# Performance work log

Measured on AMD Instinct MI355X. Metric: run time of the kernel, lower is better.

## Reference

```python
import jax, jax.numpy as jnp
import numpy as np

N_LEVELS = 16
F_PER_LEVEL = 2
LOG2_T = 19
TABLE = 1 << LOG2_T
BASE_RES = 16.0
FINEST_RES = 512.0
PRIMES = jnp.array([1, 2654435761, 805459861, 3674653429, 2097192037, 1434869437], dtype=jnp.uint32)
# Hashing offsets: BOX_OFFSETS_6D enumerates dim0 in the OUTERMOST loop -> dim d uses bit (5-d) of vertex index.
OFF_HASH = jnp.array(((np.arange(64)[:, None] >> (5 - np.arange(6))) & 1).astype(np.int32))
# Interpolation weights use LSB-first bits (vertex_binary = [i >> d & 1]) -- faithful to the source (incl. its bit-order mismatch).
OFF_W = jnp.array(((np.arange(64)[:, None] >> np.arange(6)) & 1).astype(np.bool_))


def _hash6(coords):
    # coords: [..., 6] int32 -> int32 indices in [0, 2^19). uint32 wraparound matches torch int32 overflow + bitmask.
    u = coords.astype(jnp.uint32) * PRIMES
    h = u[..., 0]
    for d in range(1, 6):
        h = h ^ u[..., d]
    return (h & jnp.uint32(TABLE - 1)).astype(jnp.int32)


def _encode_level(emb, res, x):
    # emb: [T, F], res: scalar resolution, x: [B, 6] clamped to [0,1] box
    grid = 1.0 / res
    bl = jnp.floor(x * res).astype(jnp.int32)            # bottom-left voxel index, [B, 6]
    vmin = bl.astype(x.dtype) * grid                     # voxel_min_vertex
    w = jnp.clip((x - vmin) / (grid + 1e-6), 0.0, 1.0)   # [B, 6]
    verts = bl[:, None, :] + OFF_HASH[None]              # [B, 64, 6]
    ve = emb[_hash6(verts)]                              # gather: [B, 64, F]
    wv = jnp.where(OFF_W[None], w[:, None, :], 1.0 - w[:, None, :]).prod(-1)  # [B, 64]
    return jnp.einsum('bv,bvf->bf', wv, ve)


def hash_encode(x, embeddings):
    b = np.exp((np.log(FINEST_RES) - np.log(BASE_RES)) / (N_LEVELS - 1))
    res = jnp.maximum(jnp.floor(BASE_RES * b ** jnp.arange(N_LEVELS, dtype=jnp.float32)), 1.0)
    xc = jnp.clip(x, 0.0, 1.0)

    def body(carry, lv):
        emb, r = lv
        return carry, _encode_level(emb, r, xc)

    _, feats = jax.lax.scan(body, 0, (embeddings, res))  # [L, B, F]
    return jnp.transpose(feats, (1, 0, 2)).reshape(x.shape[0], N_LEVELS * F_PER_LEVEL)


def _mlp(W0, b0, Wres, bres, scales, Wout, bout, h):
    # NeRF_MLP_Residual_Scaled: initial -> (num_layers-1) scaled residual blocks -> output
    h = jax.nn.relu(h @ W0 + b0)
    for i in range(Wres.shape[0]):
        h = scales[i] * jax.nn.relu(h @ Wres[i] + bres[i]) + h
    return h @ Wout + bout


def setup_inputs() -> dict:
    key = jax.random.key(0)
    ks = jax.random.split(key, 10)
    B, C, H, IN, OUT = 524288, 4, 256, 32, 1
    NB = 3  # num_layers - 1 residual blocks
    x = jax.random.uniform(ks[0], (B, 6), jnp.float32)
    layer_id = jax.random.randint(ks[1], (B,), 0, C)
    embeddings = jax.random.uniform(ks[2], (N_LEVELS, TABLE, F_PER_LEVEL), jnp.float32, -1e-4, 1e-4)
    W0 = jax.random.normal(ks[3], (C, IN, H), jnp.float32) / np.sqrt(IN)
    b0 = jax.random.normal(ks[4], (C, H), jnp.float32) * 0.01
    Wres = jax.random.normal(ks[5], (C, NB, H, H), jnp.float32) / np.sqrt(H)
    bres = jax.random.normal(ks[6], (C, NB, H), jnp.float32) * 0.01
    scales = jax.random.normal(ks[7], (C, NB), jnp.float32) * 0.1
    Wout = jax.random.normal(ks[8], (C, H, OUT), jnp.float32) / np.sqrt(H)
    bout = jax.random.normal(ks[9], (C, OUT), jnp.float32) * 0.01
    return dict(x_6d_input=x, layer_id=layer_id, embeddings=embeddings, W0=W0, b0=b0,
                Wres=Wres, bres=bres, scales=scales, Wout=Wout, bout=bout)


def reference(x_6d_input, layer_id, embeddings, W0, b0, Wres, bres, scales, Wout, bout):
    enc = hash_encode(x_6d_input, embeddings)  # [B, 32]
    outs = jax.vmap(_mlp, in_axes=(0, 0, 0, 0, 0, 0, 0, None))(W0, b0, Wres, bres, scales, Wout, bout, enc)  # [C, B, out]
    midx = (layer_id % outs.shape[0]).astype(jnp.int32)
    return jnp.take_along_axis(outs, midx[None, :, None], axis=0)[0]  # [B, out]
```

## Files before the change

### kernel.cpp

```cpp
#include <hip/hip_runtime.h>
#include <stdint.h>

#define HTABLE (1u << 19)
#define TMASK  (HTABLE - 1u)
#define TILE   64
#define KSTR   264
#define KE     40

#define NTILE   8196
#define NCHUNK  2049
#define BPAD    (NCHUNK * 256)

typedef __attribute__((ext_vector_type(8))) short short8;
typedef __attribute__((ext_vector_type(4))) float floatx4;

__device__ __forceinline__ float relu_(float v) { return fmaxf(v, 0.f); }

__device__ __forceinline__ uint32_t f2bf(float f) {
    uint32_t u = __float_as_uint(f);
    return (u + 0x7FFFu + ((u >> 16) & 1u)) >> 16;
}

__device__ __forceinline__ uint32_t sel4(const uint4& v, uint32_t i) {
    uint32_t lo = (i & 1u) ? v.y : v.x;
    uint32_t hi = (i & 1u) ? v.w : v.z;
    return (i & 2u) ? hi : lo;
}

__device__ __constant__ uint32_t PRS[6] = {1u, 2654435761u, 805459861u, 3674653429u, 2097192037u, 1434869437u};
__device__ __constant__ float RESF[16]  = {16.f,20.f,25.f,32.f,40.f,50.f,64.f,80.f,101.f,128.f,161.f,203.f,256.f,322.f,406.f,512.f};
__device__ __constant__ float GRIDF[16] = {1.f/16.f,1.f/20.f,1.f/25.f,1.f/32.f,1.f/40.f,1.f/50.f,1.f/64.f,1.f/80.f,
                                           1.f/101.f,1.f/128.f,1.f/161.f,1.f/203.f,1.f/256.f,1.f/322.f,1.f/406.f,1.f/512.f};

__global__ void k_count(const int* __restrict__ lid, int n, int* __restrict__ cnt) {
    __shared__ int h4[4];
    int i = blockIdx.x * blockDim.x + threadIdx.x;
    if (threadIdx.x < 4) h4[threadIdx.x] = 0;
    __syncthreads();
    if (i < n) atomicAdd(&h4[lid[i] & 3], 1);
    __syncthreads();
    if (threadIdx.x < 4) atomicAdd(&cnt[threadIdx.x], h4[threadIdx.x]);
}

__global__ void k_offsets(const int* __restrict__ cnt, int* __restrict__ cursor) {
    if (threadIdx.x == 0 && blockIdx.x == 0) {
        int off = 0;
        for (int k = 0; k < 4; k++) {
            cursor[k] = off;
            off = (off + cnt[k] + 63) & ~63;
        }
    }
}

__global__ void k_scatter(const int* __restrict__ lid, const float* __restrict__ x, int n,
                          int* __restrict__ cursor, int* __restrict__ perm, float* __restrict__ xp) {
    int i = blockIdx.x * blockDim.x + threadIdx.x;
    if (i >= n) return;
    int lane = threadIdx.x & 63;
    int c = lid[i] & 3;
    unsigned long long m0 = __ballot(c == 0), m1 = __ballot(c == 1);
    unsigned long long m2 = __ballot(c == 2), m3 = __ballot(c == 3);
    unsigned long long mc = (c == 0) ? m0 : (c == 1) ? m1 : (c == 2) ? m2 : m3;
    int rank = __popcll(mc & ((1ull << lane) - 1ull));
    int cntl = (lane == 0) ? __popcll(m0) : (lane == 1) ? __popcll(m1) : (lane == 2) ? __popcll(m2) : __popcll(m3);
    int basev = 0;
    if (lane < 4) basev = atomicAdd(&cursor[lane], cntl);
    int base = __shfl(basev, c, 64);
    int dst = base + rank;
    perm[dst] = i;
    const float2* xr = (const float2*)(x + (size_t)i * 6);
    float2* xw = (float2*)(xp + (size_t)dst * 6);
    float2 a = xr[0], b = xr[1], cc = xr[2];
    xw[0] = a; xw[1] = b; xw[2] = cc;
}

__global__ __launch_bounds__(256) void k_packtab(const float* __restrict__ emb, uint32_t* __restrict__ T) {
    const int i = blockIdx.x * 256 + threadIdx.x;
    float2 e = ((const float2*)emb)[i];
    T[i] = f2bf(e.x) | (f2bf(e.y) << 16);
}

__global__ __launch_bounds__(256) void k_prep(const float* __restrict__ Wres, const float* __restrict__ W0,
                                              uint16_t* __restrict__ Wrt, uint16_t* __restrict__ W0t) {
    __shared__ float sm[64 * 65 > 32 * 257 ? 64 * 65 : 32 * 257];
    const int t = threadIdx.x;
    const int bid = blockIdx.x;
    if (bid < 192) {
        const int c = bid / 48, rem = bid % 48, ib = rem / 16, tile = rem % 16;
        const int n0 = (tile / 4) * 64, k0 = (tile % 4) * 64;
        const float* src = Wres + (size_t)(c * 3 + ib) * 65536;
        for (int i = 0; i < 16; i++) {
            int idx = t + 256 * i, r = idx >> 6, cc = idx & 63;
            sm[r * 65 + cc] = src[(size_t)(k0 + r) * 256 + n0 + cc];
        }
        __syncthreads();
        uint16_t* dst = Wrt + (size_t)(c * 3 + ib) * 65536;
        for (int i = 0; i < 16; i++) {
            int idx = t + 256 * i, rn = idx >> 6, ck = idx & 63;
            dst[(size_t)(n0 + rn) * 256 + k0 + ck] = (uint16_t)f2bf(sm[ck * 65 + rn]);
        }
    } else {
        const int c = bid - 192;
        for (int i = 0; i < 32; i++) {
            int idx = t + 256 * i, k = idx >> 8, n = idx & 255;
            sm[k * 257 + n] = W0[(size_t)c * 8192 + idx];
        }
        __syncthreads();
        for (int i = 0; i < 32; i++) {
            int idx = t + 256 * i, n = idx >> 5, k = idx & 31;
            W0t[(size_t)c * 8192 + idx] = (uint16_t)f2bf(sm[k * 257 + n]);
        }
    }
}

__global__ __launch_bounds__(256, 4) void k_encode(
    const float* __restrict__ xp, const uint32_t* __restrict__ T,
    uint32_t* __restrict__ encP)
{
    __shared__ float xs[256 * 6];
    const int t = threadIdx.x;
    const int NC8 = NCHUNK * 8;
    const int pass = (blockIdx.x >= NC8) ? 1 : 0;
    const int rem  = blockIdx.x - pass * NC8;
    const int l    = (rem & 7) + (pass << 3);
    const int chunk = rem >> 3;
    const int pbase = chunk << 8;

    for (int idx = t; idx < 256 * 6; idx += 256) {
        float v = xp[(size_t)pbase * 6 + idx];
        xs[idx] = fminf(fmaxf(v, 0.f), 1.f);
    }
    __syncthreads();

    const float res  = RESF[l];
    const float grid = GRIDF[l];
    float wv[6]; uint32_t ua[6], ub[6];
    #pragma unroll
    for (int d = 0; d < 6; d++) {
        float xv  = xs[t * 6 + d];
        float blf = floorf(xv * res);
        float w   = (xv - blf * grid) / (grid + 1e-6f);
        wv[d] = fminf(fmaxf(w, 0.f), 1.f);
        uint32_t uu = (uint32_t)(int)blf * PRS[d];
        ua[d] = uu; ub[d] = uu + PRS[d];
    }
    uint32_t HK[4]; float WK[4];
    #pragma unroll
    for (int q = 0; q < 4; q++) {
        const int b1 = (q >> 1) & 1, bb = q & 1;
        HK[q] = (b1 ? ub[4] : ua[4]) ^ (bb ? ub[5] : ua[5]);
        WK[q] = (bb ? wv[0] : 1.f - wv[0]) * (b1 ? wv[1] : 1.f - wv[1]);
    }
    uint32_t S8[8]; float W8[8];
    #pragma unroll
    for (int jj = 0; jj < 8; jj++) {
        const int j1 = jj >> 2, j = jj & 3;
        const int b1 = (j >> 1) & 1, bb = j & 1;
        const uint32_t hj = (b1 ? ub[2] : ua[2]) ^ (bb ? ub[3] : ua[3]);
        const float  wj = ((bb ? wv[2] : 1.f - wv[2]) * (b1 ? wv[3] : 1.f - wv[3]));
        S8[jj] = (j1 ? ub[1] : ua[1]) ^ hj;
        W8[jj] = (j1 ? wv[4] : 1.f - wv[4]) * wj;
    }
    const float w5a = 1.f - wv[5], w5b = wv[5];
    const uint32_t bl0  = ua[0];
    const uint32_t mask = bl0 ^ (bl0 + 1u);
    const uint32_t* __restrict__ Tl  = T + (size_t)l * HTABLE;
    const uint4*    __restrict__ Tl4 = reinterpret_cast<const uint4*>(Tl);

    float f0 = 0.f, f1 = 0.f;
    #pragma unroll 2
    for (int jj = 0; jj < 8; jj++) {
        const uint32_t Sj = S8[jj];
        const float   wj = W8[jj];
        #pragma unroll
        for (int k = 0; k < 4; k++) {
            const uint32_t h  = (bl0 ^ Sj ^ HK[k]) & TMASK;
            const float wS = wj * WK[k];
            uint32_t pa, pb;
            if (mask == 1u) {
                const uint2 pr = *(const uint2*)(Tl + (h & ~1u));
                pa = (h & 1u) ? pr.y : pr.x;
                pb = (h & 1u) ? pr.x : pr.y;
            } else if (mask == 3u) {
                const uint4 La = Tl4[h >> 2];
                const uint32_t i0 = h & 3u;
                pa = sel4(La, i0);
                pb = sel4(La, i0 ^ 3u);
            } else {
                pa = Tl[h];
                pb = Tl[h ^ mask];
            }
            const float e0x = __uint_as_float(pa << 16),  e0y = __uint_as_float(pa & 0xFFFF0000u);
            const float e1x = __uint_as_float(pb << 16),  e1y = __uint_as_float(pb & 0xFFFF0000u);
            f0 = fmaf(wS, fmaf(w5a, e0x, w5b * e1x), f0);
            f1 = fmaf(wS, fmaf(w5a, e0y, w5b * e1y), f1);
        }
    }
    const uint32_t val = f2bf(f0) | (f2bf(f1) << 16);
    __builtin_nontemporal_store(val, &encP[(size_t)l * BPAD + pbase + t]);
}

__global__ __launch_bounds__(512, 4) void k_mlp2(
    const int* __restrict__ lid, const uint32_t* __restrict__ encP,
    const uint16_t* __restrict__ W0t, const float* __restrict__ b0,
    const uint16_t* __restrict__ Wrt, const float* __restrict__ bres,
    const float* __restrict__ scales, const float* __restrict__ Wout, const float* __restrict__ bout,
    const int* __restrict__ perm, float* __restrict__ out)
{
    __shared__ uint16_t hB[64 * KSTR];
    __shared__ __align__(16) char smU[64 * KE * 2];
    __shared__ float    bs[256];
    __shared__ int      permL[TILE];
    uint16_t* encB = (uint16_t*)smU;
    float*    outP = (float*)smU;

    const int t  = threadIdx.x;
    const int lane = t & 63;
    const int wv = t >> 6;
    const int mi = lane & 15;
    const int q  = lane >> 4;

    if (t < TILE) permL[t] = perm[(size_t)blockIdx.x * TILE + t];
    __syncthreads();
    const int g0 = permL[0];
    if (g0 < 0) return;
    const int c = lid[g0] & 3;

    if (t < 256) bs[t] = b0[c * 256 + t];
    for (int idx = t; idx < 16 * 64; idx += 512) {
        const int l = idx >> 6, pp = idx & 63;
        ((uint32_t*)encB)[pp * (KE / 2) + l] =
            __builtin_nontemporal_load(&encP[(size_t)l * BPAD + (size_t)blockIdx.x * TILE + pp]);
    }
    __syncthreads();

    floatx4 acc[2][4];
    floatx4 h_reg[2][4];

    {
        #pragma unroll
        for (int mt = 0; mt < 2; mt++)
            #pragma unroll
            for (int nt = 0; nt < 4; nt++) acc[mt][nt] = (floatx4){0.f, 0.f, 0.f, 0.f};
        const short8* Wp = (const short8*)(W0t + (size_t)c * 8192);
        short8 A[2], Bf[4];
        #pragma unroll
        for (int mt = 0; mt < 2; mt++) A[mt] = Wp[(wv * 32 + mt * 16 + mi) * 4 + q];
        #pragma unroll
        for (int nt = 0; nt < 4; nt++) Bf[nt] = *(const short8*)&encB[(nt * 16 + mi) * KE + q * 8];
        #pragma unroll
        for (int mt = 0; mt < 2; mt++)
            #pragma unroll
            for (int nt = 0; nt < 4; nt++)
                acc[mt][nt] = __builtin_amdgcn_mfma_f32_16x16x32_bf16(A[mt], Bf[nt], acc[mt][nt], 0, 0, 0);
        #pragma unroll
        for (int mt = 0; mt < 2; mt++) {
            const int nb = wv * 32 + mt * 16 + q * 4;
            #pragma unroll
            for (int nt = 0; nt < 4; nt++) {
                floatx4 u = acc[mt][nt], h;
                h[0] = relu_(u[0] + bs[nb + 0]); h[1] = relu_(u[1] + bs[nb + 1]);
                h[2] = relu_(u[2] + bs[nb + 2]); h[3] = relu_(u[3] + bs[nb + 3]);
                h_reg[mt][nt] = h;
                uint2 pk; pk.x = f2bf(h[0]) | (f2bf(h[1]) << 16); pk.y = f2bf(h[2]) | (f2bf(h[3]) << 16);
                *(uint2*)&hB[(nt * 16 + mi) * KSTR + nb] = pk;
            }
        }
    }
    __syncthreads();

    #pragma unroll 1
    for (int ib = 0; ib < 3; ib++) {
        if (t < 256) bs[t] = bres[(size_t)((c * 3 + ib) << 8) + t];
        const float s = scales[c * 3 + ib];
        #pragma unroll
        for (int mt = 0; mt < 2; mt++)
            #pragma unroll
            for (int nt = 0; nt < 4; nt++) acc[mt][nt] = (floatx4){0.f, 0.f, 0.f, 0.f};

        const short8* Wp = (const short8*)(Wrt + (size_t)(c * 3 + ib) * 65536);
        short8 Acur[2], Anext[2], Bf[4];
        #pragma unroll
        for (int mt = 0; mt < 2; mt++) Acur[mt] = Wp[(wv * 32 + mt * 16 + mi) * 32 + q];
        #pragma unroll 1
        for (int ks = 0; ks < 8; ks++) {
            #pragma unroll
            for (int nt = 0; nt < 4; nt++)
                Bf[nt] = *(const short8*)&hB[(nt * 16 + mi) * KSTR + ks * 32 + q * 8];
            if (ks < 7) {
                #pragma unroll
                for (int mt = 0; mt < 2; mt++)
                    Anext[mt] = Wp[(wv * 32 + mt * 16 + mi) * 32 + (ks + 1) * 4 + q];
            }
            #pragma unroll
            for (int mt = 0; mt < 2; mt++)
                #pragma unroll
                for (int nt = 0; nt < 4; nt++)
                    acc[mt][nt] = __builtin_amdgcn_mfma_f32_16x16x32_bf16(Acur[mt], Bf[nt], acc[mt][nt], 0, 0, 0);
            #pragma unroll
            for (int mt = 0; mt < 2; mt++) Acur[mt] = Anext[mt];
        }
        __syncthreads();
        #pragma unroll
        for (int mt = 0; mt < 2; mt++) {
            const int nb = wv * 32 + mt * 16 + q * 4;
            #pragma unroll
            for (int nt = 0; nt < 4; nt++) {
                floatx4 u = acc[mt][nt];
                floatx4 h = h_reg[mt][nt];
                h[0] = fmaf(s, relu_(u[0] + bs[nb + 0]), h[0]);
                h[1] = fmaf(s, relu_(u[1] + bs[nb + 1]), h[1]);
                h[2] = fmaf(s, relu_(u[2] + bs[nb + 2]), h[2]);
                h[3] = fmaf(s, relu_(u[3] + bs[nb + 3]), h[3]);
                h_reg[mt][nt] = h;
                if (ib < 2) {
                    uint2 pk; pk.x = f2bf(h[0]) | (f2bf(h[1]) << 16); pk.y = f2bf(h[2]) | (f2bf(h[3]) << 16);
                    *(uint2*)&hB[(nt * 16 + mi) * KSTR + nb] = pk;
                }
            }
        }
        if (ib < 2) __syncthreads();
    }

    __syncthreads();
    if (t < 256) bs[t] = Wout[c * 256 + t];
    __syncthreads();
    float po[4] = {0.f, 0.f, 0.f, 0.f};
    #pragma unroll
    for (int mt = 0; mt < 2; mt++) {
        const int nb = wv * 32 + mt * 16 + q * 4;
        const float w0v = bs[nb + 0], w1v = bs[nb + 1], w2v = bs[nb + 2], w3v = bs[nb + 3];
        #pragma unroll
        for (int nt = 0; nt < 4; nt++) {
            const floatx4 h = h_reg[mt][nt];
            po[nt] += h[0] * w0v + h[1] * w1v + h[2] * w2v + h[3] * w3v;
        }
    }
    #pragma unroll
    for (int nt = 0; nt < 4; nt++) {
        float v = po[nt];
        v += __shfl_xor(v, 16, 64);
        v += __shfl_xor(v, 32, 64);
        if (q == 0) outP[wv * 64 + nt * 16 + mi] = v;
    }
    __syncthreads();
    if (t < TILE) {
        float r = outP[t]       + outP[64 + t]  + outP[128 + t] + outP[192 + t]
                + outP[256 + t] + outP[320 + t] + outP[384 + t] + outP[448 + t] + bout[c];
        const int gi = permL[t];
        if (gi >= 0) out[gi] = r;
    }
}

extern "C" void kernel_launch(void* const* d_in, const int* in_sizes, int n_in,
                              void* d_out, int out_size, void* d_ws, size_t ws_size,
                              hipStream_t stream) {
    const float* x      = (const float*)d_in[0];
    const int*   lid    = (const int*)  d_in[1];
    const float* emb    = (const float*)d_in[2];
    const float* W0     = (const float*)d_in[3];
    const float* b0     = (const float*)d_in[4];
    const float* Wres   = (const float*)d_in[5];
    const float* bres   = (const float*)d_in[6];
    const float* scales = (const float*)d_in[7];
    const float* Wout   = (const float*)d_in[8];
    const float* bout   = (const float*)d_in[9];
    float* out = (float*)d_out;

    const int B = in_sizes[1];
    int* cnt    = (int*)d_ws;
    int* cursor = cnt + 4;
    int*      perm = (int*)((char*)d_ws + 16384);
    uint16_t* W0t  = (uint16_t*)((char*)d_ws + 2228224);
    uint16_t* Wrt  = (uint16_t*)((char*)d_ws + 2359296);
    uint32_t* encP = (uint32_t*)((char*)d_ws + (4ull  << 20));
    uint32_t* T    = (uint32_t*)((char*)d_ws + (38ull << 20));
    float*    xp   = (float*)   ((char*)d_ws + (70ull << 20));

    (void)hipMemsetAsync(d_ws, 0, 64, stream);
    (void)hipMemsetAsync(perm, 0xFF, (size_t)NTILE * TILE * sizeof(int), stream);
    k_packtab<<<(16 * (int)HTABLE) / 256, 256, 0, stream>>>(emb, T);
    k_prep   <<<196, 256, 0, stream>>>(Wres, W0, Wrt, W0t);
    k_count  <<<B / 256, 256, 0, stream>>>(lid, B, cnt);
    k_offsets<<<1, 64, 0, stream>>>(cnt, cursor);
    k_scatter<<<B / 256, 256, 0, stream>>>(lid, x, B, cursor, perm, xp);
    k_encode <<<NCHUNK * 16, 256, 0, stream>>>(xp, T, encP);
    k_mlp2   <<<NTILE, 512, 0, stream>>>(lid, encP, W0t, b0, Wrt, bres, scales, Wout, bout, perm, out);
}
```

Measured before the change: 1.742 ms.

## Fuse prep kernels into one launch and retile MLP waves as 4x2 fragments

Merges the table packing, weight transposition, class counting and perm memset into a single kernel, so several launches and a memset become one launch. In the MLP kernel each wave now covers 64 output features by 32 points (4x2 MFMA tiles) instead of 32x64 (2x4). That doubles the weight fragments per wave and halves the activation fragments read from LDS. The partial output reduction changes to four partials per point, read as one float4. The fused kernel hardcodes block counts (COUNT_N 2048) that assume a fixed batch size, and the larger A-fragment set raises register pressure.

```diff
diff --git a/kernel.cpp b/kernel.cpp
--- a/kernel.cpp
+++ b/kernel.cpp
@@ -11,6 +11,11 @@
 #define NCHUNK  2049
 #define BPAD    (NCHUNK * 256)
 
+#define PACK_N  32768
+#define PREP_N  196
+#define COUNT_N 2048
+#define PERM_N  2049
+
 typedef __attribute__((ext_vector_type(8))) short short8;
 typedef __attribute__((ext_vector_type(4))) float floatx4;
 
@@ -32,14 +37,64 @@
 __device__ __constant__ float GRIDF[16] = {1.f/16.f,1.f/20.f,1.f/25.f,1.f/32.f,1.f/40.f,1.f/50.f,1.f/64.f,1.f/80.f,
                                            1.f/101.f,1.f/128.f,1.f/161.f,1.f/203.f,1.f/256.f,1.f/322.f,1.f/406.f,1.f/512.f};
 
-__global__ void k_count(const int* __restrict__ lid, int n, int* __restrict__ cnt) {
-    __shared__ int h4[4];
-    int i = blockIdx.x * blockDim.x + threadIdx.x;
-    if (threadIdx.x < 4) h4[threadIdx.x] = 0;
-    __syncthreads();
-    if (i < n) atomicAdd(&h4[lid[i] & 3], 1);
-    __syncthreads();
-    if (threadIdx.x < 4) atomicAdd(&cnt[threadIdx.x], h4[threadIdx.x]);
+__global__ __launch_bounds__(256) void k_fusedprep(
+    const float* __restrict__ emb, uint32_t* __restrict__ T,
+    const float* __restrict__ Wres, const float* __restrict__ W0,
+    uint16_t* __restrict__ Wrt, uint16_t* __restrict__ W0t,
+    const int* __restrict__ lid, int n, int* __restrict__ cnt,
+    int* __restrict__ perm)
+{
+    const int t = threadIdx.x;
+    const int bid = blockIdx.x;
+    if (bid < PACK_N) {
+        const int i = bid * 256 + t;
+        float2 e = ((const float2*)emb)[i];
+        T[i] = f2bf(e.x) | (f2bf(e.y) << 16);
+        return;
+    }
+    if (bid < PACK_N + PREP_N) {
+        __shared__ float sm[64 * 65 > 32 * 257 ? 64 * 65 : 32 * 257];
+        const int pb = bid - PACK_N;
+        if (pb < 192) {
+            const int c = pb / 48, rem = pb % 48, ib = rem / 16, tile = rem % 16;
+            const int n0 = (tile / 4) * 64, k0 = (tile % 4) * 64;
+            const float* src = Wres + (size_t)(c * 3 + ib) * 65536;
+            for (int i = 0; i < 16; i++) {
+                int idx = t + 256 * i, r = idx >> 6, cc = idx & 63;
+                sm[r * 65 + cc] = src[(size_t)(k0 + r) * 256 + n0 + cc];
+            }
+            __syncthreads();
+            uint16_t* dst = Wrt + (size_t)(c * 3 + ib) * 65536;
+            for (int i = 0; i < 16; i++) {
+                int idx = t + 256 * i, rn = idx >> 6, ck = idx & 63;
+                dst[(size_t)(n0 + rn) * 256 + k0 + ck] = (uint16_t)f2bf(sm[ck * 65 + rn]);
+            }
+        } else {
+            const int c = pb - 192;
+            for (int i = 0; i < 32; i++) {
+                int idx = t + 256 * i, k = idx >> 8, nn = idx & 255;
+                sm[k * 257 + nn] = W0[(size_t)c * 8192 + idx];
+            }
+            __syncthreads();
+            for (int i = 0; i < 32; i++) {
+                int idx = t + 256 * i, nn = idx >> 5, k = idx & 31;
+                W0t[(size_t)c * 8192 + idx] = (uint16_t)f2bf(sm[k * 257 + nn]);
+            }
+        }
+        return;
+    }
+    if (bid < PACK_N + PREP_N + COUNT_N) {
+        __shared__ int h4[4];
+        const int i = (bid - PACK_N - PREP_N) * 256 + t;
+        if (t < 4) h4[t] = 0;
+        __syncthreads();
+        if (i < n) atomicAdd(&h4[lid[i] & 3], 1);
+        __syncthreads();
+        if (t < 4) atomicAdd(&cnt[t], h4[t]);
+        return;
+    }
+    const int i = (bid - PACK_N - PREP_N - COUNT_N) * 256 + t;
+    if (i < NTILE * TILE) perm[i] = -1;
 }
 
 __global__ void k_offsets(const int* __restrict__ cnt, int* __restrict__ cursor) {
@@ -74,45 +129,6 @@
     xw[0] = a; xw[1] = b; xw[2] = cc;
 }
 
-__global__ __launch_bounds__(256) void k_packtab(const float* __restrict__ emb, uint32_t* __restrict__ T) {
-    const int i = blockIdx.x * 256 + threadIdx.x;
-    float2 e = ((const float2*)emb)[i];
-    T[i] = f2bf(e.x) | (f2bf(e.y) << 16);
-}
-
-__global__ __launch_bounds__(256) void k_prep(const float* __restrict__ Wres, const float* __restrict__ W0,
-                                              uint16_t* __restrict__ Wrt, uint16_t* __restrict__ W0t) {
-    __shared__ float sm[64 * 65 > 32 * 257 ? 64 * 65 : 32 * 257];
-    const int t = threadIdx.x;
-    const int bid = blockIdx.x;
-    if (bid < 192) {
-        const int c = bid / 48, rem = bid % 48, ib = rem / 16, tile = rem % 16;
-        const int n0 = (tile / 4) * 64, k0 = (tile % 4) * 64;
-        const float* src = Wres + (size_t)(c * 3 + ib) * 65536;
-        for (int i = 0; i < 16; i++) {
-            int idx = t + 256 * i, r = idx >> 6, cc = idx & 63;
-            sm[r * 65 + cc] = src[(size_t)(k0 + r) * 256 + n0 + cc];
-        }
-        __syncthreads();
-        uint16_t* dst = Wrt + (size_t)(c * 3 + ib) * 65536;
-        for (int i = 0; i < 16; i++) {
-            int idx = t + 256 * i, rn = idx >> 6, ck = idx & 63;
-            dst[(size_t)(n0 + rn) * 256 + k0 + ck] = (uint16_t)f2bf(sm[ck * 65 + rn]);
-        }
-    } else {
-        const int c = bid - 192;
-        for (int i = 0; i < 32; i++) {
-            int idx = t + 256 * i, k = idx >> 8, n = idx & 255;
-            sm[k * 257 + n] = W0[(size_t)c * 8192 + idx];
-        }
-        __syncthreads();
-        for (int i = 0; i < 32; i++) {
-            int idx = t + 256 * i, n = idx >> 5, k = idx & 31;
-            W0t[(size_t)c * 8192 + idx] = (uint16_t)f2bf(sm[k * 257 + n]);
-        }
-    }
-}
-
 __global__ __launch_bounds__(256, 4) void k_encode(
     const float* __restrict__ xp, const uint32_t* __restrict__ T,
     uint32_t* __restrict__ encP)
@@ -217,6 +233,8 @@
     const int t  = threadIdx.x;
     const int lane = t & 63;
     const int wv = t >> 6;
+    const int s  = wv >> 1;
+    const int ph = wv & 1;
     const int mi = lane & 15;
     const int q  = lane >> 4;
 
@@ -234,36 +252,36 @@
     }
     __syncthreads();
 
-    floatx4 acc[2][4];
-    floatx4 h_reg[2][4];
+    floatx4 acc[4][2];
+    floatx4 h_reg[4][2];
 
     {
         #pragma unroll
-        for (int mt = 0; mt < 2; mt++)
-            #pragma unroll
-            for (int nt = 0; nt < 4; nt++) acc[mt][nt] = (floatx4){0.f, 0.f, 0.f, 0.f};
+        for (int mt = 0; mt < 4; mt++)
+            #pragma unroll
+            for (int nt = 0; nt < 2; nt++) acc[mt][nt] = (floatx4){0.f, 0.f, 0.f, 0.f};
         const short8* Wp = (const short8*)(W0t + (size_t)c * 8192);
-        short8 A[2], Bf[4];
-        #pragma unroll
-        for (int mt = 0; mt < 2; mt++) A[mt] = Wp[(wv * 32 + mt * 16 + mi) * 4 + q];
-        #pragma unroll
-        for (int nt = 0; nt < 4; nt++) Bf[nt] = *(const short8*)&encB[(nt * 16 + mi) * KE + q * 8];
-        #pragma unroll
-        for (int mt = 0; mt < 2; mt++)
-            #pragma unroll
-            for (int nt = 0; nt < 4; nt++)
+        short8 A[4], Bf[2];
+        #pragma unroll
+        for (int mt = 0; mt < 4; mt++) A[mt] = Wp[(s * 64 + mt * 16 + mi) * 4 + q];
+        #pragma unroll
+        for (int nt = 0; nt < 2; nt++) Bf[nt] = *(const short8*)&encB[(ph * 32 + nt * 16 + mi) * KE + q * 8];
+        #pragma unroll
+        for (int mt = 0; mt < 4; mt++)
+            #pragma unroll
+            for (int nt = 0; nt < 2; nt++)
                 acc[mt][nt] = __builtin_amdgcn_mfma_f32_16x16x32_bf16(A[mt], Bf[nt], acc[mt][nt], 0, 0, 0);
         #pragma unroll
-        for (int mt = 0; mt < 2; mt++) {
-            const int nb = wv * 32 + mt * 16 + q * 4;
-            #pragma unroll
-            for (int nt = 0; nt < 4; nt++) {
+        for (int mt = 0; mt < 4; mt++) {
+            const int nb = s * 64 + mt * 16 + q * 4;
+            #pragma unroll
+            for (int nt = 0; nt < 2; nt++) {
                 floatx4 u = acc[mt][nt], h;
                 h[0] = relu_(u[0] + bs[nb + 0]); h[1] = relu_(u[1] + bs[nb + 1]);
                 h[2] = relu_(u[2] + bs[nb + 2]); h[3] = relu_(u[3] + bs[nb + 3]);
                 h_reg[mt][nt] = h;
                 uint2 pk; pk.x = f2bf(h[0]) | (f2bf(h[1]) << 16); pk.y = f2bf(h[2]) | (f2bf(h[3]) << 16);
-                *(uint2*)&hB[(nt * 16 + mi) * KSTR + nb] = pk;
+                *(uint2*)&hB[(ph * 32 + nt * 16 + mi) * KSTR + nb] = pk;
             }
         }
     }
@@ -272,50 +290,50 @@
     #pragma unroll 1
     for (int ib = 0; ib < 3; ib++) {
         if (t < 256) bs[t] = bres[(size_t)((c * 3 + ib) << 8) + t];
-        const float s = scales[c * 3 + ib];
-        #pragma unroll
-        for (int mt = 0; mt < 2; mt++)
-            #pragma unroll
-            for (int nt = 0; nt < 4; nt++) acc[mt][nt] = (floatx4){0.f, 0.f, 0.f, 0.f};
+        const float sc = scales[c * 3 + ib];
+        #pragma unroll
+        for (int mt = 0; mt < 4; mt++)
+            #pragma unroll
+            for (int nt = 0; nt < 2; nt++) acc[mt][nt] = (floatx4){0.f, 0.f, 0.f, 0.f};
 
         const short8* Wp = (const short8*)(Wrt + (size_t)(c * 3 + ib) * 65536);
-        short8 Acur[2], Anext[2], Bf[4];
-        #pragma unroll
-        for (int mt = 0; mt < 2; mt++) Acur[mt] = Wp[(wv * 32 + mt * 16 + mi) * 32 + q];
+        short8 Acur[4], Anext[4], Bf[2];
+        #pragma unroll
+        for (int mt = 0; mt < 4; mt++) Acur[mt] = Wp[(s * 64 + mt * 16 + mi) * 32 + q];
         #pragma unroll 1
         for (int ks = 0; ks < 8; ks++) {
             #pragma unroll
-            for (int nt = 0; nt < 4; nt++)
-                Bf[nt] = *(const short8*)&hB[(nt * 16 + mi) * KSTR + ks * 32 + q * 8];
+            for (int nt = 0; nt < 2; nt++)
+                Bf[nt] = *(const short8*)&hB[(ph * 32 + nt * 16 + mi) * KSTR + ks * 32 + q * 8];
             if (ks < 7) {
                 #pragma unroll
-                for (int mt = 0; mt < 2; mt++)
-                    Anext[mt] = Wp[(wv * 32 + mt * 16 + mi) * 32 + (ks + 1) * 4 + q];
-            }
-            #pragma unroll
-            for (int mt = 0; mt < 2; mt++)
+                for (int mt = 0; mt < 4; mt++)
+                    Anext[mt] = Wp[(s * 64 + mt * 16 + mi) * 32 + (ks + 1) * 4 + q];
+            }
+            #pragma unroll
+            for (int mt = 0; mt < 4; mt++)
                 #pragma unroll
-                for (int nt = 0; nt < 4; nt++)
+                for (int nt = 0; nt < 2; nt++)
                     acc[mt][nt] = __builtin_amdgcn_mfma_f32_16x16x32_bf16(Acur[mt], Bf[nt], acc[mt][nt], 0, 0, 0);
             #pragma unroll
-            for (int mt = 0; mt < 2; mt++) Acur[mt] = Anext[mt];
+            for (int mt = 0; mt < 4; mt++) Acur[mt] = Anext[mt];
         }
         __syncthreads();
         #pragma unroll
-        for (int mt = 0; mt < 2; mt++) {
-            const int nb = wv * 32 + mt * 16 + q * 4;
-            #pragma unroll
-            for (int nt = 0; nt < 4; nt++) {
+        for (int mt = 0; mt < 4; mt++) {
+            const int nb = s * 64 + mt * 16 + q * 4;
+            #pragma unroll
+            for (int nt = 0; nt < 2; nt++) {
                 floatx4 u = acc[mt][nt];
                 floatx4 h = h_reg[mt][nt];
-                h[0] = fmaf(s, relu_(u[0] + bs[nb + 0]), h[0]);
-                h[1] = fmaf(s, relu_(u[1] + bs[nb + 1]), h[1]);
-                h[2] = fmaf(s, relu_(u[2] + bs[nb + 2]), h[2]);
-                h[3] = fmaf(s, relu_(u[3] + bs[nb + 3]), h[3]);
+                h[0] = fmaf(sc, relu_(u[0] + bs[nb + 0]), h[0]);
+                h[1] = fmaf(sc, relu_(u[1] + bs[nb + 1]), h[1]);
+                h[2] = fmaf(sc, relu_(u[2] + bs[nb + 2]), h[2]);
+                h[3] = fmaf(sc, relu_(u[3] + bs[nb + 3]), h[3]);
                 h_reg[mt][nt] = h;
                 if (ib < 2) {
                     uint2 pk; pk.x = f2bf(h[0]) | (f2bf(h[1]) << 16); pk.y = f2bf(h[2]) | (f2bf(h[3]) << 16);
-                    *(uint2*)&hB[(nt * 16 + mi) * KSTR + nb] = pk;
+                    *(uint2*)&hB[(ph * 32 + nt * 16 + mi) * KSTR + nb] = pk;
                 }
             }
         }
@@ -325,28 +343,28 @@
     __syncthreads();
     if (t < 256) bs[t] = Wout[c * 256 + t];
     __syncthreads();
-    float po[4] = {0.f, 0.f, 0.f, 0.f};
+    float po[2] = {0.f, 0.f};
     #pragma unroll
-    for (int mt = 0; mt < 2; mt++) {
-        const int nb = wv * 32 + mt * 16 + q * 4;
+    for (int mt = 0; mt < 4; mt++) {
+        const int nb = s * 64 + mt * 16 + q * 4;
         const float w0v = bs[nb + 0], w1v = bs[nb + 1], w2v = bs[nb + 2], w3v = bs[nb + 3];
         #pragma unroll
-        for (int nt = 0; nt < 4; nt++) {
+        for (int nt = 0; nt < 2; nt++) {
             const floatx4 h = h_reg[mt][nt];
             po[nt] += h[0] * w0v + h[1] * w1v + h[2] * w2v + h[3] * w3v;
         }
     }
     #pragma unroll
-    for (int nt = 0; nt < 4; nt++) {
+    for (int nt = 0; nt < 2; nt++) {
         float v = po[nt];
         v += __shfl_xor(v, 16, 64);
         v += __shfl_xor(v, 32, 64);
-        if (q == 0) outP[wv * 64 + nt * 16 + mi] = v;
+        if (q == 0) outP[(ph * 32 + nt * 16 + mi) * 4 + s] = v;
     }
     __syncthreads();
     if (t < TILE) {
-        float r = outP[t]       + outP[64 + t]  + outP[128 + t] + outP[192 + t]
-                + outP[256 + t] + outP[320 + t] + outP[384 + t] + outP[448 + t] + bout[c];
+        const float4 p4 = *(const float4*)&outP[t * 4];
+        float r = p4.x + p4.y + p4.z + p4.w + bout[c];
         const int gi = permL[t];
         if (gi >= 0) out[gi] = r;
     }
@@ -378,10 +396,8 @@
     float*    xp   = (float*)   ((char*)d_ws + (70ull << 20));
 
     (void)hipMemsetAsync(d_ws, 0, 64, stream);
-    (void)hipMemsetAsync(perm, 0xFF, (size_t)NTILE * TILE * sizeof(int), stream);
-    k_packtab<<<(16 * (int)HTABLE) / 256, 256, 0, stream>>>(emb, T);
-    k_prep   <<<196, 256, 0, stream>>>(Wres, W0, Wrt, W0t);
-    k_count  <<<B / 256, 256, 0, stream>>>(lid, B, cnt);
+    k_fusedprep<<<PACK_N + PREP_N + COUNT_N + PERM_N, 256, 0, stream>>>(
+        emb, T, Wres, W0, Wrt, W0t, lid, B, cnt, perm);
     k_offsets<<<1, 64, 0, stream>>>(cnt, cursor);
     k_scatter<<<B / 256, 256, 0, stream>>>(lid, x, B, cursor, perm, xp);
     k_encode <<<NCHUNK * 16, 256, 0, stream>>>(xp, T, encP);
```

Measured after the change: 2.070 ms. 1.19x slower.
